# Kernel optimization log

Measured on AMD Instinct MI355X. Metric: run time of the kernel, lower is better.

The kernel has to match this reference:

```python
import jax, jax.numpy as jnp
import numpy as np
from jax import lax

N_KCS = 5000
B = 512
T = 100

def setup_inputs() -> dict:
    key = jax.random.key(0)
    k1, k2, k3, k4 = jax.random.split(key, 4)
    prev_kc = jax.random.randint(k1, (B, T), 0, N_KCS, dtype=jnp.int32)
    curr_kc = jax.random.randint(k2, (B, T), 0, N_KCS, dtype=jnp.int32)
    prev_corr = jax.random.randint(k3, (B, T), 0, 2, dtype=jnp.int32)
    kc_logits = jax.random.normal(k4, (N_KCS, 5), dtype=jnp.float32)  # nn.Embedding(n_kcs, 5)
    return {"prev_kc": prev_kc, "curr_kc": curr_kc, "prev_corr": prev_corr, "kc_logits": kc_logits}


def reference(prev_kc, curr_kc, prev_corr, kc_logits):
    n_batch, t = prev_kc.shape
    batch_ix = jnp.arange(n_batch)
    probs_tbl = jax.nn.sigmoid(kc_logits)  # [K,5]: learn, forget, guess(p|h=0), slip-comp(p|h=1), init

    # ---- first trial: state = tile of sigmoid(logits[:,4]) ----
    state0 = jnp.tile(probs_tbl[:, 4][None, :], (n_batch, 1))  # [B, K]
    curr_p0 = probs_tbl[curr_kc[:, 0]]                          # [B, 5]
    cs0 = state0[batch_ix, curr_kc[:, 0]]
    pc0 = curr_p0[:, 2] * (1.0 - cs0) + curr_p0[:, 3] * cs0      # [B]

    def step(state, inp):
        pk, ck, pcorr = inp                      # each [B]
        prev_p = probs_tbl[pk]                   # [B,5]
        curr_p = probs_tbl[ck]                   # [B,5]
        c = pcorr.astype(state.dtype)[:, None]   # [B,1]
        pch = prev_p[:, 2:4]                     # p(correct | h=0/1)
        p_out = jnp.power(pch, c) * jnp.power(1.0 - pch, 1.0 - c)  # [B,2]
        skill = state[batch_ix, pk]
        filt = p_out[:, 1] * skill / (p_out[:, 0] * (1.0 - skill) + p_out[:, 1] * skill)
        predictive = prev_p[:, 0] * (1.0 - filt) + (1.0 - prev_p[:, 1]) * filt
        state = state.at[batch_ix, pk].set(predictive)
        cs = state[batch_ix, ck]
        p_curr = curr_p[:, 2] * (1.0 - cs) + curr_p[:, 3] * cs
        return state, p_curr

    xs = (prev_kc[:, 1:].T, curr_kc[:, 1:].T, prev_corr[:, 1:].T)  # [T-1, B]
    state_f, pcs = lax.scan(step, state0, xs)                       # pcs: [T-1, B]
    probs = jnp.concatenate([pc0[:, None], pcs.T], axis=1)          # [B, T]
    return probs, state_f
```

## Files before the change

kernel.cpp:

```cpp
#include <hip/hip_runtime.h>
#include <math.h>

#define N_KCS 5000
#define TT    100
#define BB    512

__device__ __forceinline__ float sigmoidf(float x) {
    return 1.0f / (1.0f + expf(-x));
}

__global__ __launch_bounds__(256) void sigmoid_tbl_kernel(
    const float* __restrict__ logits,
    float*       __restrict__ tbl,
    float*       __restrict__ init_tbl)
{
    int i = blockIdx.x * 256 + threadIdx.x;
    if (i < N_KCS * 5) {
        float s = sigmoidf(logits[i]);
        tbl[i] = s;
        if (i % 5 == 4) init_tbl[i / 5] = s;
    }
}

__global__ __launch_bounds__(256) void bkt_kernel(
    const int*   __restrict__ prev_kc,
    const int*   __restrict__ curr_kc,
    const int*   __restrict__ prev_corr,
    const float* __restrict__ tbl,
    const float* __restrict__ init_tbl,
    float*       __restrict__ probs_out,
    float*       __restrict__ state_out)
{
    __shared__ float state[N_KCS];
    __shared__ int   pk_s[TT], ck_s[TT], nxt_s[TT];
    __shared__ float po0_s[TT], po1_s[TT], pp0_s[TT], pp1_s[TT];
    __shared__ float cp2_s[TT], cp3_s[TT], pred_s[TT];

    const int b    = blockIdx.x;
    const int tid  = threadIdx.x;
    const int base = b * TT;

    if (tid < TT) {
        pk_s[tid] = prev_kc[base + tid];
        ck_s[tid] = curr_kc[base + tid];
    }
    for (int k = tid * 4; k < N_KCS; k += 256 * 4) {
        *(float4*)&state[k] = *(const float4*)&init_tbl[k];
    }
    __syncthreads();

    const int  t   = tid;
    const bool act = (t >= 1 && t < TT);
    int  lst  = -1;
    bool head = true;

    if (act) {
        const int mypk = pk_s[t];
        const int myck = ck_s[t];
        const int c    = prev_corr[base + t];

        float pp2 = tbl[mypk * 5 + 2];
        float pp3 = tbl[mypk * 5 + 3];
        pp0_s[t] = tbl[mypk * 5 + 0];
        pp1_s[t] = tbl[mypk * 5 + 1];
        cp2_s[t] = tbl[myck * 5 + 2];
        cp3_s[t] = tbl[myck * 5 + 3];
        po0_s[t] = c ? pp2 : (1.0f - pp2);
        po1_s[t] = c ? pp3 : (1.0f - pp3);

        int nxt = -1;
        for (int tp = 1; tp < TT; ++tp) {
            int p = pk_s[tp];
            if (p == mypk) {
                if (tp < t)                    head = false;
                else if (tp > t && nxt == -1)  nxt  = tp;
            }
            if (p == myck && tp <= t) lst = tp;
        }
        nxt_s[t] = nxt;
    }

    if (t == 0) {
        int   ck0 = ck_s[0];
        float cs0 = state[ck0];
        probs_out[base] = tbl[ck0 * 5 + 2] * (1.0f - cs0) + tbl[ck0 * 5 + 3] * cs0;
    }
    __syncthreads();

    if (act && head) {
        float s = state[pk_s[t]];
        int   u = t;
        while (u != -1) {
            float num        = po1_s[u] * s;
            float filt       = num / (po0_s[u] * (1.0f - s) + num);
            float predictive = pp0_s[u] * (1.0f - filt) + (1.0f - pp1_s[u]) * filt;
            pred_s[u] = predictive;
            s = predictive;
            u = nxt_s[u];
        }
    }
    __syncthreads();

    if (act) {
        float cs = (lst == -1) ? state[ck_s[t]] : pred_s[lst];
        probs_out[base + t] = cp2_s[t] * (1.0f - cs) + cp3_s[t] * cs;
    }
    __syncthreads();

    if (act && nxt_s[t] == -1) {
        state[pk_s[t]] = pred_s[t];
    }
    __syncthreads();

    float* out_row = state_out + (size_t)b * N_KCS;
    for (int k = tid * 4; k < N_KCS; k += 256 * 4) {
        *(float4*)&out_row[k] = *(const float4*)&state[k];
    }
}

extern "C" void kernel_launch(void* const* d_in, const int* in_sizes, int n_in,
                              void* d_out, int out_size, void* d_ws, size_t ws_size,
                              hipStream_t stream) {
    const int*   prev_kc   = (const int*)d_in[0];
    const int*   curr_kc   = (const int*)d_in[1];
    const int*   prev_corr = (const int*)d_in[2];
    const float* logits    = (const float*)d_in[3];

    float* tbl      = (float*)d_ws;
    float* init_tbl = tbl + 25024;

    float* out     = (float*)d_out;
    float* probs   = out;
    float* state_f = out + BB * TT;

    sigmoid_tbl_kernel<<<(N_KCS * 5 + 255) / 256, 256, 0, stream>>>(
        logits, tbl, init_tbl);
    bkt_kernel<<<BB, 256, 0, stream>>>(prev_kc, curr_kc, prev_corr,
                                       tbl, init_tbl, probs, state_f);
}
```

Before: 76.79 us.

## Fuse sigmoid table into BKT kernel and drop shared-memory state array

Removes the separate sigmoid table kernel and computes sigmoids from the logits on the fly inside the main kernel. The 20KB shared state array goes away: the output row is written straight from the init sigmoids, then the final predictive values are scattered over it after a barrier. This saves a launch and the table round trip, and the smaller shared footprint allows more resident blocks. In exchange each block recomputes 5000 sigmoids with strided loads of the logits, and correctness depends on the scatter landing after the block's own row writes, which the barrier orders.

```diff
diff --git a/kernel.cpp b/kernel.cpp
--- a/kernel.cpp
+++ b/kernel.cpp
@@ -9,29 +9,14 @@
     return 1.0f / (1.0f + expf(-x));
 }
 
-__global__ __launch_bounds__(256) void sigmoid_tbl_kernel(
-    const float* __restrict__ logits,
-    float*       __restrict__ tbl,
-    float*       __restrict__ init_tbl)
-{
-    int i = blockIdx.x * 256 + threadIdx.x;
-    if (i < N_KCS * 5) {
-        float s = sigmoidf(logits[i]);
-        tbl[i] = s;
-        if (i % 5 == 4) init_tbl[i / 5] = s;
-    }
-}
-
-__global__ __launch_bounds__(256) void bkt_kernel(
+__global__ __launch_bounds__(256) void bkt_fused_kernel(
     const int*   __restrict__ prev_kc,
     const int*   __restrict__ curr_kc,
     const int*   __restrict__ prev_corr,
-    const float* __restrict__ tbl,
-    const float* __restrict__ init_tbl,
+    const float* __restrict__ logits,
     float*       __restrict__ probs_out,
     float*       __restrict__ state_out)
 {
-    __shared__ float state[N_KCS];
     __shared__ int   pk_s[TT], ck_s[TT], nxt_s[TT];
     __shared__ float po0_s[TT], po1_s[TT], pp0_s[TT], pp1_s[TT];
     __shared__ float cp2_s[TT], cp3_s[TT], pred_s[TT];
@@ -44,29 +29,28 @@
         pk_s[tid] = prev_kc[base + tid];
         ck_s[tid] = curr_kc[base + tid];
     }
-    for (int k = tid * 4; k < N_KCS; k += 256 * 4) {
-        *(float4*)&state[k] = *(const float4*)&init_tbl[k];
-    }
     __syncthreads();
 
     const int  t   = tid;
     const bool act = (t >= 1 && t < TT);
-    int  lst  = -1;
-    bool head = true;
+    int   lst     = -1;
+    bool  head    = true;
+    float init_pk = 0.0f;
 
     if (act) {
         const int mypk = pk_s[t];
         const int myck = ck_s[t];
         const int c    = prev_corr[base + t];
 
-        float pp2 = tbl[mypk * 5 + 2];
-        float pp3 = tbl[mypk * 5 + 3];
-        pp0_s[t] = tbl[mypk * 5 + 0];
-        pp1_s[t] = tbl[mypk * 5 + 1];
-        cp2_s[t] = tbl[myck * 5 + 2];
-        cp3_s[t] = tbl[myck * 5 + 3];
-        po0_s[t] = c ? pp2 : (1.0f - pp2);
-        po1_s[t] = c ? pp3 : (1.0f - pp3);
+        float pp2 = sigmoidf(logits[mypk * 5 + 2]);
+        float pp3 = sigmoidf(logits[mypk * 5 + 3]);
+        pp0_s[t]  = sigmoidf(logits[mypk * 5 + 0]);
+        pp1_s[t]  = sigmoidf(logits[mypk * 5 + 1]);
+        cp2_s[t]  = sigmoidf(logits[myck * 5 + 2]);
+        cp3_s[t]  = sigmoidf(logits[myck * 5 + 3]);
+        po0_s[t]  = c ? pp2 : (1.0f - pp2);
+        po1_s[t]  = c ? pp3 : (1.0f - pp3);
+        init_pk   = sigmoidf(logits[mypk * 5 + 4]);
 
         int nxt = -1;
         for (int tp = 1; tp < TT; ++tp) {
@@ -82,13 +66,14 @@
 
     if (t == 0) {
         int   ck0 = ck_s[0];
-        float cs0 = state[ck0];
-        probs_out[base] = tbl[ck0 * 5 + 2] * (1.0f - cs0) + tbl[ck0 * 5 + 3] * cs0;
+        float cs0 = sigmoidf(logits[ck0 * 5 + 4]);
+        probs_out[base] = sigmoidf(logits[ck0 * 5 + 2]) * (1.0f - cs0)
+                        + sigmoidf(logits[ck0 * 5 + 3]) * cs0;
     }
     __syncthreads();
 
     if (act && head) {
-        float s = state[pk_s[t]];
+        float s = init_pk;
         int   u = t;
         while (u != -1) {
             float num        = po1_s[u] * s;
@@ -102,19 +87,23 @@
     __syncthreads();
 
     if (act) {
-        float cs = (lst == -1) ? state[ck_s[t]] : pred_s[lst];
+        float cs = (lst == -1) ? sigmoidf(logits[ck_s[t] * 5 + 4]) : pred_s[lst];
         probs_out[base + t] = cp2_s[t] * (1.0f - cs) + cp3_s[t] * cs;
+    }
+
+    float* out_row = state_out + (size_t)b * N_KCS;
+    for (int k4 = tid * 4; k4 < N_KCS; k4 += 256 * 4) {
+        float4 v;
+        v.x = sigmoidf(logits[(k4 + 0) * 5 + 4]);
+        v.y = sigmoidf(logits[(k4 + 1) * 5 + 4]);
+        v.z = sigmoidf(logits[(k4 + 2) * 5 + 4]);
+        v.w = sigmoidf(logits[(k4 + 3) * 5 + 4]);
+        *(float4*)&out_row[k4] = v;
     }
     __syncthreads();
 
     if (act && nxt_s[t] == -1) {
-        state[pk_s[t]] = pred_s[t];
-    }
-    __syncthreads();
-
-    float* out_row = state_out + (size_t)b * N_KCS;
-    for (int k = tid * 4; k < N_KCS; k += 256 * 4) {
-        *(float4*)&out_row[k] = *(const float4*)&state[k];
+        out_row[pk_s[t]] = pred_s[t];
     }
 }
 
@@ -126,15 +115,10 @@
     const int*   prev_corr = (const int*)d_in[2];
     const float* logits    = (const float*)d_in[3];
 
-    float* tbl      = (float*)d_ws;
-    float* init_tbl = tbl + 25024;
-
     float* out     = (float*)d_out;
     float* probs   = out;
     float* state_f = out + BB * TT;
 
-    sigmoid_tbl_kernel<<<(N_KCS * 5 + 255) / 256, 256, 0, stream>>>(
-        logits, tbl, init_tbl);
-    bkt_kernel<<<BB, 256, 0, stream>>>(prev_kc, curr_kc, prev_corr,
-                                       tbl, init_tbl, probs, state_f);
+    bkt_fused_kernel<<<BB, 256, 0, stream>>>(prev_kc, curr_kc, prev_corr,
+                                             logits, probs, state_f);
 }
```

New measurement: 75.75 us. No clear change (-1.4%).
